# Performance work log

Measured on AMD Instinct MI355X. Metric: run time of the kernel, lower is better.

The kernel has to match this reference:

```python
import jax, jax.numpy as jnp
import numpy as np

D_K = 64  # key/query head dim used for the 1/sqrt(d_k) scale


def setup_inputs() -> dict:
    key0 = jax.random.key(0)
    kk, kq, kv = jax.random.split(key0, 3)
    B, H, S, DK, DV = 2, 16, 2048, 64, 64
    return {
        "key": jax.random.normal(kk, (B, H, S, DK), dtype=jnp.float32),
        "query": jax.random.normal(kq, (B, H, S, DK), dtype=jnp.float32),
        "value": jax.random.normal(kv, (B, H, S, DV), dtype=jnp.float32),
    }


def reference(key, query, value):
    # scaled dot-product attention per head: [B,H,S,S]
    scores = jnp.einsum("bhqd,bhkd->bhqk", query, key) / jnp.sqrt(jnp.asarray(D_K, query.dtype))
    attn = jax.nn.softmax(scores, axis=-1)
    out = jnp.einsum("bhqk,bhkv->bhqv", attn, value)  # [B,H,S,d_v]
    B, H, S, DV = out.shape
    # faithful to the torch .view: raw reshape (no head transpose)
    return out.reshape(B, S, H * DV)
```

## Files before the change

### kernel.cpp

```cpp
#include <hip/hip_runtime.h>

#define S_LEN 2048
#define DHEAD 64
#define BHEADS 32
#define NTILES 32
#define HEAD_ELEMS (S_LEN * DHEAD)
#define TENS_ELEMS (BHEADS * HEAD_ELEMS)
#define TILE_HALVES 4096

typedef _Float16 half8_t __attribute__((ext_vector_type(8)));
typedef _Float16 half4_t __attribute__((ext_vector_type(4)));
typedef _Float16 half2_t __attribute__((ext_vector_type(2)));
typedef float float4_t __attribute__((ext_vector_type(4)));

#define SC_LOG2E 0.18033688011112042f


__global__ __launch_bounds__(256) void prep_kernel(const float* __restrict__ K,
                                                   const float* __restrict__ V,
                                                   _Float16* __restrict__ Kf,
                                                   _Float16* __restrict__ Vf) {
    __shared__ _Float16 tile[64][72];
    const int bh = blockIdx.x >> 5;
    const int t = blockIdx.x & 31;
    const int tid = threadIdx.x;

    const float* Ksrc = K + (bh * S_LEN + t * 64) * DHEAD;
    const float4* vs = (const float4*)(V + (bh * S_LEN + t * 64) * DHEAD);
#pragma unroll
    for (int it = 0; it < 4; ++it) {
        int i = it * 256 + tid;
        float4 vv = vs[i];
        int r = i >> 4, c4 = (i & 15) * 4;
        half4_t hv = {(_Float16)vv.x, (_Float16)vv.y, (_Float16)vv.z, (_Float16)vv.w};
        *(half4_t*)&tile[r][c4] = hv;
    }

    _Float16* kd = Kf + (bh * NTILES + t) * TILE_HALVES;
#pragma unroll
    for (int it = 0; it < 2; ++it) {
        int c = it * 256 + tid;
        int f = c >> 6, lane = c & 63;
        int row = (f >> 1) * 16 + (lane & 15);
        int d0 = (f & 1) * 32 + (lane >> 4) * 8;
        const float4* s = (const float4*)(Ksrc + row * DHEAD + d0);
        float4 a = s[0], b = s[1];
        half8_t h = {(_Float16)(a.x * SC_LOG2E), (_Float16)(a.y * SC_LOG2E),
                     (_Float16)(a.z * SC_LOG2E), (_Float16)(a.w * SC_LOG2E),
                     (_Float16)(b.x * SC_LOG2E), (_Float16)(b.y * SC_LOG2E),
                     (_Float16)(b.z * SC_LOG2E), (_Float16)(b.w * SC_LOG2E)};
        *(half8_t*)(kd + c * 8) = h;
    }
    __syncthreads();

    _Float16* vd = Vf + (bh * NTILES + t) * TILE_HALVES;
#pragma unroll
    for (int it = 0; it < 2; ++it) {
        int c = it * 256 + tid;
        int fv = c >> 6, lane = c & 63;
        int vt = fv >> 1, ktp = fv & 1;
        int v = vt * 16 + (lane & 15);
        int g = lane >> 4;
        half8_t h;
#pragma unroll
        for (int j = 0; j < 8; ++j) {
            int key = ktp * 32 + (j >> 2) * 16 + g * 4 + (j & 3);
            h[j] = tile[key][v];
        }
        *(half8_t*)(vd + c * 8) = h;
    }
}


__global__ __launch_bounds__(256, 2) void attn_kernel(
    const float* __restrict__ Qf,
    const _Float16* __restrict__ Kf,
    const _Float16* __restrict__ Vf,
    float* __restrict__ out) {
    __shared__ float red[2][68][64];

    const int tid = threadIdx.x;
    const int wid = tid >> 6;
    const int lane = tid & 63;
    const int ln15 = lane & 15;
    const int g = lane >> 4;

    const int bh = blockIdx.x >> 4;
    const int qpair = blockIdx.x & 15;
    const int qg = wid >> 1;
    const int ks = wid & 1;
    const int q0 = qpair * 128 + qg * 64;
    const int t0 = ks * 16;

    const float* Qg = Qf + (bh * S_LEN + q0) * DHEAD;
    half8_t qf[4][2];
#pragma unroll
    for (int nq = 0; nq < 4; ++nq)
#pragma unroll
        for (int kh = 0; kh < 2; ++kh) {
            const float4* qs = (const float4*)(Qg + (nq * 16 + ln15) * DHEAD + kh * 32 + g * 8);
            float4 a = qs[0], b = qs[1];
            qf[nq][kh] = (half8_t){(_Float16)a.x, (_Float16)a.y, (_Float16)a.z, (_Float16)a.w,
                                   (_Float16)b.x, (_Float16)b.y, (_Float16)b.z, (_Float16)b.w};
        }

    const _Float16* kb = Kf + bh * (NTILES * TILE_HALVES) + t0 * TILE_HALVES;
    const _Float16* vb = Vf + bh * (NTILES * TILE_HALVES) + t0 * TILE_HALVES;
    const int lo = lane * 8;

    half8_t kf[2][8], vf[2][8];
#pragma unroll
    for (int f = 0; f < 8; ++f) {
        kf[0][f] = *(const half8_t*)(kb + f * 512 + lo);
        vf[0][f] = *(const half8_t*)(vb + f * 512 + lo);
    }

    float lsum[4] = {0.f, 0.f, 0.f, 0.f};
    float4_t o[4][4];
#pragma unroll
    for (int nq = 0; nq < 4; ++nq)
#pragma unroll
        for (int vt = 0; vt < 4; ++vt) o[nq][vt] = (float4_t){0.f, 0.f, 0.f, 0.f};

#pragma unroll 2
    for (int t = 0; t < 16; ++t) {
        const int cur = t & 1;
        const int tn = (t + 1 < 16) ? t + 1 : t;
        const _Float16* kbn = kb + tn * TILE_HALVES;
        const _Float16* vbn = vb + tn * TILE_HALVES;
#pragma unroll
        for (int f = 0; f < 8; ++f) {
            kf[cur ^ 1][f] = *(const half8_t*)(kbn + f * 512 + lo);
            vf[cur ^ 1][f] = *(const half8_t*)(vbn + f * 512 + lo);
        }

#pragma unroll
        for (int ktp = 0; ktp < 2; ++ktp) {
            half4_t pb[4][2];
#pragma unroll
            for (int mh = 0; mh < 2; ++mh) {
                const int mt = ktp * 2 + mh;
                half8_t a0 = kf[cur][mt * 2];
                half8_t a1 = kf[cur][mt * 2 + 1];
#pragma unroll
                for (int nq = 0; nq < 4; ++nq) {
                    float4_t c0 = (float4_t){0.f, 0.f, 0.f, 0.f};
                    c0 = __builtin_amdgcn_mfma_f32_16x16x32_f16(a0, qf[nq][0], c0, 0, 0, 0);
                    c0 = __builtin_amdgcn_mfma_f32_16x16x32_f16(a1, qf[nq][1], c0, 0, 0, 0);
                    float p0 = __builtin_amdgcn_exp2f(c0[0]);
                    float p1 = __builtin_amdgcn_exp2f(c0[1]);
                    float p2 = __builtin_amdgcn_exp2f(c0[2]);
                    float p3 = __builtin_amdgcn_exp2f(c0[3]);
                    lsum[nq] += (p0 + p1) + (p2 + p3);
                    half2_t plo = __builtin_bit_cast(half2_t, __builtin_amdgcn_cvt_pkrtz(p0, p1));
                    half2_t phi = __builtin_bit_cast(half2_t, __builtin_amdgcn_cvt_pkrtz(p2, p3));
                    pb[nq][mh] = (half4_t){plo[0], plo[1], phi[0], phi[1]};
                }
            }
#pragma unroll
            for (int vt = 0; vt < 4; ++vt) {
                half8_t va = vf[cur][vt * 2 + ktp];
                half4_t alo = __builtin_shufflevector(va, va, 0, 1, 2, 3);
                half4_t ahi = __builtin_shufflevector(va, va, 4, 5, 6, 7);
#pragma unroll
                for (int nq = 0; nq < 4; ++nq) {
                    o[nq][vt] = __builtin_amdgcn_mfma_f32_16x16x16f16(alo, pb[nq][0], o[nq][vt], 0, 0, 0);
                    o[nq][vt] = __builtin_amdgcn_mfma_f32_16x16x16f16(ahi, pb[nq][1], o[nq][vt], 0, 0, 0);
                }
            }
        }
    }

#pragma unroll
    for (int nq = 0; nq < 4; ++nq) {
        float l = lsum[nq];
        l += __shfl_xor(l, 16, 64);
        l += __shfl_xor(l, 32, 64);
        lsum[nq] = l;
    }

    if (ks == 1) {
#pragma unroll
        for (int nq = 0; nq < 4; ++nq)
#pragma unroll
            for (int vt = 0; vt < 4; ++vt)
#pragma unroll
                for (int r = 0; r < 4; ++r)
                    red[qg][nq * 16 + vt * 4 + r][lane] = o[nq][vt][r];
#pragma unroll
        for (int nq = 0; nq < 4; ++nq) red[qg][64 + nq][lane] = lsum[nq];
    }
    __syncthreads();
    if (ks == 0) {
#pragma unroll
        for (int nq = 0; nq < 4; ++nq) {
            float lt = lsum[nq] + red[qg][64 + nq][lane];
            float inv_l = 1.0f / lt;
            int qg_global = q0 + nq * 16 + ln15;
            float* og = out + (bh * S_LEN + qg_global) * DHEAD;
#pragma unroll
            for (int vt = 0; vt < 4; ++vt) {
                float4_t vals;
#pragma unroll
                for (int r = 0; r < 4; ++r)
                    vals[r] = (o[nq][vt][r] + red[qg][nq * 16 + vt * 4 + r][lane]) * inv_l;
                *(float4_t*)(og + vt * 16 + g * 4) = vals;
            }
        }
    }
}


extern "C" void kernel_launch(void* const* d_in, const int* in_sizes, int n_in,
                              void* d_out, int out_size, void* d_ws, size_t ws_size,
                              hipStream_t stream) {
    const float* Kin = (const float*)d_in[0];
    const float* Qin = (const float*)d_in[1];
    const float* Vin = (const float*)d_in[2];
    float* out = (float*)d_out;

    _Float16* Kf = (_Float16*)d_ws;
    _Float16* Vf = Kf + TENS_ELEMS;

    prep_kernel<<<BHEADS * NTILES, 256, 0, stream>>>(Kin, Vin, Kf, Vf);
    attn_kernel<<<BHEADS * 16, 256, 0, stream>>>(Qin, Kf, Vf, out);
}
```

Before: 152.7 us.

## Use 16x16x32 MFMA for PV, drop register double-buffering, interleave heads across blocks

The P·V product now uses one 16x16x32 f16 MFMA per tile instead of two 16x16x16 MFMAs. The probability fragments from two QK^T sub-tiles are packed into one 8-wide vector, relying on the existing V fragment layout to line up the K dimension. The explicit register double-buffered prefetch of K/V tiles is removed in favour of plain per-iteration loads, which cuts register pressure but exposes load latency unless the compiler or the second resident block hides it. Block indexing also changes so that consecutive blocks cover different heads rather than different query chunks of the same head, which alters L2 locality of the shared K/V.

```diff
diff --git a/kernel.cpp b/kernel.cpp
--- a/kernel.cpp
+++ b/kernel.cpp
@@ -85,11 +85,11 @@
     const int ln15 = lane & 15;
     const int g = lane >> 4;
 
-    const int bh = blockIdx.x >> 4;
-    const int qpair = blockIdx.x & 15;
+    const int bh = blockIdx.x & 31;
+    const int qidx = blockIdx.x >> 5;
     const int qg = wid >> 1;
     const int ks = wid & 1;
-    const int q0 = qpair * 128 + qg * 64;
+    const int q0 = qidx * 128 + qg * 64;
     const int t0 = ks * 16;
 
     const float* Qg = Qf + (bh * S_LEN + q0) * DHEAD;
@@ -108,13 +108,6 @@
     const _Float16* vb = Vf + bh * (NTILES * TILE_HALVES) + t0 * TILE_HALVES;
     const int lo = lane * 8;
 
-    half8_t kf[2][8], vf[2][8];
-#pragma unroll
-    for (int f = 0; f < 8; ++f) {
-        kf[0][f] = *(const half8_t*)(kb + f * 512 + lo);
-        vf[0][f] = *(const half8_t*)(vb + f * 512 + lo);
-    }
-
     float lsum[4] = {0.f, 0.f, 0.f, 0.f};
     float4_t o[4][4];
 #pragma unroll
@@ -124,24 +117,21 @@
 
 #pragma unroll 2
     for (int t = 0; t < 16; ++t) {
-        const int cur = t & 1;
-        const int tn = (t + 1 < 16) ? t + 1 : t;
-        const _Float16* kbn = kb + tn * TILE_HALVES;
-        const _Float16* vbn = vb + tn * TILE_HALVES;
-#pragma unroll
-        for (int f = 0; f < 8; ++f) {
-            kf[cur ^ 1][f] = *(const half8_t*)(kbn + f * 512 + lo);
-            vf[cur ^ 1][f] = *(const half8_t*)(vbn + f * 512 + lo);
-        }
-
-#pragma unroll
-        for (int ktp = 0; ktp < 2; ++ktp) {
-            half4_t pb[4][2];
-#pragma unroll
-            for (int mh = 0; mh < 2; ++mh) {
-                const int mt = ktp * 2 + mh;
-                half8_t a0 = kf[cur][mt * 2];
-                half8_t a1 = kf[cur][mt * 2 + 1];
+        const int base = t * TILE_HALVES;
+        half8_t kf[8], vf[8];
+#pragma unroll
+        for (int f = 0; f < 8; ++f) kf[f] = *(const half8_t*)(kb + base + f * 512 + lo);
+#pragma unroll
+        for (int f = 0; f < 8; ++f) vf[f] = *(const half8_t*)(vb + base + f * 512 + lo);
+
+#pragma unroll
+        for (int c = 0; c < 2; ++c) {
+            half8_t pb[4];
+#pragma unroll
+            for (int h = 0; h < 2; ++h) {
+                const int mt = 2 * c + h;
+                half8_t a0 = kf[mt * 2];
+                half8_t a1 = kf[mt * 2 + 1];
 #pragma unroll
                 for (int nq = 0; nq < 4; ++nq) {
                     float4_t c0 = (float4_t){0.f, 0.f, 0.f, 0.f};
@@ -154,19 +144,18 @@
                     lsum[nq] += (p0 + p1) + (p2 + p3);
                     half2_t plo = __builtin_bit_cast(half2_t, __builtin_amdgcn_cvt_pkrtz(p0, p1));
                     half2_t phi = __builtin_bit_cast(half2_t, __builtin_amdgcn_cvt_pkrtz(p2, p3));
-                    pb[nq][mh] = (half4_t){plo[0], plo[1], phi[0], phi[1]};
+                    pb[nq][h * 4 + 0] = plo[0];
+                    pb[nq][h * 4 + 1] = plo[1];
+                    pb[nq][h * 4 + 2] = phi[0];
+                    pb[nq][h * 4 + 3] = phi[1];
                 }
             }
 #pragma unroll
             for (int vt = 0; vt < 4; ++vt) {
-                half8_t va = vf[cur][vt * 2 + ktp];
-                half4_t alo = __builtin_shufflevector(va, va, 0, 1, 2, 3);
-                half4_t ahi = __builtin_shufflevector(va, va, 4, 5, 6, 7);
-#pragma unroll
-                for (int nq = 0; nq < 4; ++nq) {
-                    o[nq][vt] = __builtin_amdgcn_mfma_f32_16x16x16f16(alo, pb[nq][0], o[nq][vt], 0, 0, 0);
-                    o[nq][vt] = __builtin_amdgcn_mfma_f32_16x16x16f16(ahi, pb[nq][1], o[nq][vt], 0, 0, 0);
-                }
+                half8_t va = vf[vt * 2 + c];
+#pragma unroll
+                for (int nq = 0; nq < 4; ++nq)
+                    o[nq][vt] = __builtin_amdgcn_mfma_f32_16x16x32_f16(va, pb[nq], o[nq][vt], 0, 0, 0);
             }
         }
     }
```

After: 127.8 us. -16.3%, faster.
